# Optimization experiments

Measured on AMD Instinct MI355X. Metric: run time of the kernel, lower is better.

The kernel has to match this reference:

```python
import jax, jax.numpy as jnp
import numpy as np

D = 128  # input_depth == output_depth
NUM_NODES_PATTERN = np.tile(np.array([32, 48, 64, 96], dtype=np.int64), 64)  # G=256 graphs


def _build_indices(nn_np):
    """Per pair-entry (row-major within each n_g x n_g block): global row node,
    global col node, graph id, diagonal mask; plus per-node graph id / size."""
    G = len(nn_np)
    offs = np.zeros(G, dtype=np.int64)
    offs[1:] = np.cumsum(nn_np)[:-1]
    rows_l, cols_l, g_l, diag_l = [], [], [], []
    for gi, (n, o) in enumerate(zip(nn_np, offs)):
        i = np.repeat(np.arange(n, dtype=np.int64), n)  # row index within block
        j = np.tile(np.arange(n, dtype=np.int64), n)    # col index within block
        rows_l.append(o + i)
        cols_l.append(o + j)
        g_l.append(np.full(n * n, gi, dtype=np.int64))
        diag_l.append(i == j)
    rows = np.concatenate(rows_l)
    cols = np.concatenate(cols_l)
    g_edge = np.concatenate(g_l)
    diag = np.concatenate(diag_l)
    g_node = np.repeat(np.arange(G, dtype=np.int64), nn_np)  # graph of each node
    n_node = np.repeat(nn_np, nn_np)                          # n_g of each node
    N = int(nn_np.sum())
    return rows, cols, g_edge, diag, g_node, n_node, N, G


def setup_inputs() -> dict:
    key = jax.random.key(0)
    nn_np = NUM_NODES_PATTERN
    E = int(np.sum(nn_np ** 2))  # 1,064,960 pair entries
    N = int(nn_np.sum())         # 15,360 nodes
    k1, k2, k3 = jax.random.split(key, 3)
    x = jax.random.normal(k1, (E, D), dtype=jnp.float32)
    coeffs = jax.random.normal(k2, (D, D, 5), dtype=jnp.float32) * float(np.sqrt(2.0) / (D + D))
    bias = jnp.zeros((1, D), dtype=jnp.float32)
    edges_index = jax.random.randint(k3, (2, E), 0, N, dtype=jnp.int64)  # unused by the layer
    num_nodes = jnp.asarray(nn_np)
    return {"x": x, "coeffs": coeffs, "bias": bias,
            "edges_index": edges_index, "num_nodes": num_nodes}


def reference(x, coeffs, bias, edges_index, num_nodes):
    # edges_index is unused, matching the original forward.
    nn_np = np.asarray(num_nodes)
    rows, cols, g_edge, diag, g_node, n_node, N, G = _build_indices(nn_np)
    seg = jax.ops.segment_sum
    diag_m = jnp.asarray(diag)[:, None].astype(x.dtype)  # [E,1]
    n = jnp.asarray(n_node).astype(x.dtype)[:, None]     # [N,1] block size per node

    op1 = seg(x * diag_m, jnp.asarray(rows), num_segments=N)          # diag part (unnormalized)
    op3 = seg(x, jnp.asarray(rows), num_segments=N) / n               # row sums / n
    op4 = seg(x, jnp.asarray(cols), num_segments=N) / n               # col sums / n
    diag_g = seg(x * diag_m, jnp.asarray(g_edge), num_segments=G)     # [G,d] trace per graph
    all_g = seg(x, jnp.asarray(g_edge), num_segments=G)               # [G,d] total sum per graph
    gn = jnp.asarray(g_node)
    op2 = diag_g[gn] / n                                              # trace broadcast / n
    op5 = all_g[gn] / (n * n)                                         # total broadcast / n^2

    ops = jnp.stack([op1, op2, op3, op4, op5], axis=2)                # [N, d, 5]
    out = jnp.einsum('dsb,ndb->ns', coeffs, ops) + bias               # [N, output_depth]
    return out
```

## Files before the change

kernel.cpp:

```cpp
#include <hip/hip_runtime.h>

#define D 128


__device__ __forceinline__ void f4add(float4& a, const float4& b) {
    a.x += b.x; a.y += b.y; a.z += b.z; a.w += b.w;
}

__device__ __forceinline__ void f4shflxor_add(float4& a, int mask) {
    a.x += __shfl_xor(a.x, mask);
    a.y += __shfl_xor(a.y, mask);
    a.z += __shfl_xor(a.z, mask);
    a.w += __shfl_xor(a.w, mask);
}

template<int N>
__device__ __forceinline__ void run_class(const float* __restrict__ x,
                                          long ebase, int o, int gidx, int chunk,
                                          float* __restrict__ diagG,
                                          float* __restrict__ rowG,
                                          float* __restrict__ colG,
                                          float* __restrict__ trG,
                                          float* __restrict__ totG,
                                          float4* rowpart ) {
    const int tid = threadIdx.x;
    const int L   = tid & 63;
    const int w   = tid >> 6;
    const int j0  = tid >> 3;
    const int f4  = tid & 7;
    const float invn = 1.0f / (float)N;
    constexpr bool TWO = (N > 64);
    const bool act0 = (j0 < N);
    const bool act1 = TWO && (j0 + 64 < N);

    const float4* x4 = reinterpret_cast<const float4*>(x);
    const long e0 = (ebase + j0) * 32 + chunk * 8 + f4;
    const long e1 = e0 + 64L * 32;
    const long istride = (long)N * 32;

    float4 c0 = {0,0,0,0}, c1 = {0,0,0,0};

    for (int t0 = 0; t0 < N; t0 += 16) {
#pragma unroll 8
        for (int r = 0; r < 16; ++r) {
            const int i = t0 + r;
            float4 v0 = {0,0,0,0}, v1 = {0,0,0,0};
            if (act0) v0 = x4[e0 + (long)i * istride];
            if (TWO && act1) v1 = x4[e1 + (long)i * istride];
            f4add(c0, v0);
            if (TWO) f4add(c1, v1);
            float4 s = v0;
            if (TWO) f4add(s, v1);
            f4shflxor_add(s, 8);
            f4shflxor_add(s, 16);
            f4shflxor_add(s, 32);
            if (L < 8) rowpart[(r * 8 + w) * 8 + L] = s;
        }
        __syncthreads();
        {
            const int r  = tid >> 5;
            const int dd = tid & 31;
            const float* rp = reinterpret_cast<const float*>(rowpart);
            float acc = 0.f;
#pragma unroll
            for (int w2 = 0; w2 < 8; ++w2) acc += rp[r * 256 + w2 * 32 + dd];
            rowG[(long)(o + t0 + r) * D + chunk * 32 + dd] = acc * invn;
        }
        __syncthreads();
    }

    float4 d0 = {0,0,0,0}, d1 = {0,0,0,0};
    if (act0) d0 = x4[e0 + (long)j0 * istride];
    if (TWO && act1) d1 = x4[e1 + (long)(j0 + 64) * istride];

    float4* diag4 = reinterpret_cast<float4*>(diagG);
    float4* col4  = reinterpret_cast<float4*>(colG);
    if (act0) {
        diag4[(long)(o + j0) * 32 + chunk * 8 + f4] = d0;
        col4 [(long)(o + j0) * 32 + chunk * 8 + f4] = c0;
    }
    if (TWO && act1) {
        diag4[(long)(o + j0 + 64) * 32 + chunk * 8 + f4] = d1;
        col4 [(long)(o + j0 + 64) * 32 + chunk * 8 + f4] = c1;
    }

    float4 td = d0; if (TWO) f4add(td, d1);
    float4 tc = c0; if (TWO) f4add(tc, c1);
    f4shflxor_add(td, 8);  f4shflxor_add(tc, 8);
    f4shflxor_add(td, 16); f4shflxor_add(tc, 16);
    f4shflxor_add(td, 32); f4shflxor_add(tc, 32);
    if (L < 8) {
        rowpart[w * 8 + L]      = td;
        rowpart[64 + w * 8 + L] = tc;
    }
    __syncthreads();
    float4* tr4  = reinterpret_cast<float4*>(trG);
    float4* tot4 = reinterpret_cast<float4*>(totG);
    if (tid < 8) {
        float4 a = {0,0,0,0};
#pragma unroll
        for (int w2 = 0; w2 < 8; ++w2) f4add(a, rowpart[w2 * 8 + tid]);
        tr4[gidx * 32 + chunk * 8 + tid] = a;
    } else if (tid < 16) {
        const int f = tid - 8;
        float4 a = {0,0,0,0};
#pragma unroll
        for (int w2 = 0; w2 < 8; ++w2) f4add(a, rowpart[64 + w2 * 8 + f]);
        tot4[gidx * 32 + chunk * 8 + f] = a;
    }
}

__global__ __launch_bounds__(512) void k1_reduce(const float* __restrict__ x,
                                                 float* __restrict__ diagG,
                                                 float* __restrict__ rowG,
                                                 float* __restrict__ colG,
                                                 float* __restrict__ trG,
                                                 float* __restrict__ totG) {
    __shared__ float4 rowpart[1024];

    const int b  = blockIdx.x;
    const int bb = b & 255;
    const int k  = bb >> 2;
    const int chunk = bb & 3;

    if (b < 256) {
        run_class<96>(x, 16640L * k + 7424, 240 * k + 144, 4 * k + 3, chunk, diagG, rowG, colG, trG, totG, rowpart);
    } else if (b < 512) {
        run_class<64>(x, 16640L * k + 3328, 240 * k + 80, 4 * k + 2, chunk, diagG, rowG, colG, trG, totG, rowpart);
    } else if (b < 768) {
        run_class<48>(x, 16640L * k + 1024, 240 * k + 32, 4 * k + 1, chunk, diagG, rowG, colG, trG, totG, rowpart);
    } else {
        run_class<32>(x, 16640L * k, 240 * k, 4 * k, chunk, diagG, rowG, colG, trG, totG, rowpart);
    }
}

__global__ void k0_transpose(const float* __restrict__ coeffs, float* __restrict__ Wt) {
    int d = blockIdx.x;
    int s = threadIdx.x;
    const float* cp = coeffs + ((long)d * D + s) * 5;
#pragma unroll
    for (int b = 0; b < 5; ++b) Wt[b * (D * D) + d * D + s] = cp[b];
}

__global__ __launch_bounds__(128) void k2_pg(const float* __restrict__ trG,
                                             const float* __restrict__ totG,
                                             const float* __restrict__ Wt,
                                             const float* __restrict__ bias,
                                             float* __restrict__ pg) {
    __shared__ float tr[D], tt[D];
    const int ns_[4] = {32, 48, 64, 96};
    int g = blockIdx.x;
    int c = g & 3;
    float invn = 1.0f / (float)ns_[c];

    int s = threadIdx.x;
    tr[s] = trG[g * D + s] * invn;
    tt[s] = totG[g * D + s] * invn * invn;
    __syncthreads();

    const float* W1 = Wt + 1 * D * D;
    const float* W4 = Wt + 4 * D * D;
    float acc = 0.f;
#pragma unroll 4
    for (int dd = 0; dd < D; ++dd)
        acc += W1[dd * D + s] * tr[dd] + W4[dd * D + s] * tt[dd];
    pg[g * D + s] = bias[s] + acc;
}

__global__ __launch_bounds__(512) void k3_gemm(const float* __restrict__ diagG,
                                               const float* __restrict__ rowG,
                                               const float* __restrict__ colG,
                                               const float* __restrict__ Wt,
                                               const float* __restrict__ pg,
                                               float* __restrict__ out) {
    __shared__ float ash[3][64][D];
    __shared__ int gish[64];
    const int nd0 = blockIdx.x * 64;
    const int tid = threadIdx.x;

    for (int idx = tid; idx < 64 * D; idx += 512) {
        int nn = idx >> 7;
        int d  = idx & 127;
        int nd = nd0 + nn;
        int p  = nd / 240;
        int r  = nd - p * 240;
        int c, n;
        if (r < 32)       { c = 0; n = 32; }
        else if (r < 80)  { c = 1; n = 48; }
        else if (r < 144) { c = 2; n = 64; }
        else              { c = 3; n = 96; }
        float invn = 1.0f / (float)n;
        ash[0][nn][d] = diagG[(long)nd * D + d];
        ash[1][nn][d] = rowG[(long)nd * D + d];
        ash[2][nn][d] = colG[(long)nd * D + d] * invn;
        if (d == 0) gish[nn] = 4 * p + c;
    }
    __syncthreads();

    const int s0 = tid & 31;
    const int nq = tid >> 5;
    const float* W0 = Wt;
    const float* W2 = Wt + 2 * D * D;
    const float* W3 = Wt + 3 * D * D;

    float acc[4][4];
#pragma unroll
    for (int a = 0; a < 4; ++a)
#pragma unroll
        for (int ss = 0; ss < 4; ++ss) acc[a][ss] = 0.f;

    for (int d = 0; d < D; ++d) {
        float w0[4], w2[4], w3[4];
#pragma unroll
        for (int ss = 0; ss < 4; ++ss) {
            int s = s0 + 32 * ss;
            w0[ss] = W0[d * D + s];
            w2[ss] = W2[d * D + s];
            w3[ss] = W3[d * D + s];
        }
#pragma unroll
        for (int a = 0; a < 4; ++a) {
            int nn = nq * 4 + a;
            float a0 = ash[0][nn][d];
            float a1 = ash[1][nn][d];
            float a2 = ash[2][nn][d];
#pragma unroll
            for (int ss = 0; ss < 4; ++ss)
                acc[a][ss] += w0[ss] * a0 + w2[ss] * a1 + w3[ss] * a2;
        }
    }

#pragma unroll
    for (int a = 0; a < 4; ++a) {
        int nn = nq * 4 + a;
        int nd = nd0 + nn;
        int g  = gish[nn];
#pragma unroll
        for (int ss = 0; ss < 4; ++ss) {
            int s = s0 + 32 * ss;
            out[(long)nd * D + s] = acc[a][ss] + pg[g * D + s];
        }
    }
}

extern "C" void kernel_launch(void* const* d_in, const int* in_sizes, int n_in,
                              void* d_out, int out_size, void* d_ws, size_t ws_size,
                              hipStream_t stream) {
    const float* x      = (const float*)d_in[0];
    const float* coeffs = (const float*)d_in[1];
    const float* bias   = (const float*)d_in[2];

    float* ws    = (float*)d_ws;
    float* Wt    = ws;
    float* diagG = Wt + 81920;
    float* rowG  = diagG + 1966080;
    float* colG  = rowG + 1966080;
    float* pg    = colG + 1966080;
    float* trG   = pg + 32768;
    float* totG  = trG + 32768;
    float* out   = (float*)d_out;

    k0_transpose<<<128, 128, 0, stream>>>(coeffs, Wt);
    k1_reduce<<<1024, 512, 0, stream>>>(x, diagG, rowG, colG, trG, totG);
    k2_pg<<<256, 128, 0, stream>>>(trG, totG, Wt, bias, pg);
    k3_gemm<<<240, 512, 0, stream>>>(diagG, rowG, colG, Wt, pg, out);
}
```

Baseline: 227.3 us.

## Replace per-tile shuffle row reduction with diagonal-skewed LDS atomic accumulation

Each thread now walks its column starting at the diagonal row and wrapping around, so lanes in a wave touch distinct rows at each step. Row sums are accumulated with shared-memory float atomics into a padded buffer, which removes the cross-lane shuffles and the two block barriers per 16-row tile. The diagonal element is captured on the first iteration. The cost is four LDS atomics per loaded vector and a less contiguous global access pattern across lanes.

```diff
diff --git a/kernel.cpp b/kernel.cpp
--- a/kernel.cpp
+++ b/kernel.cpp
@@ -22,56 +22,80 @@
                                           float* __restrict__ colG,
                                           float* __restrict__ trG,
                                           float* __restrict__ totG,
-                                          float4* rowpart ) {
+                                          float* __restrict__ rowacc ,
+                                          float4* __restrict__ red   ) {
     const int tid = threadIdx.x;
+    const int j0  = tid >> 3;
+    const int f4  = tid & 7;
     const int L   = tid & 63;
     const int w   = tid >> 6;
-    const int j0  = tid >> 3;
-    const int f4  = tid & 7;
-    const float invn = 1.0f / (float)N;
     constexpr bool TWO = (N > 64);
     const bool act0 = (j0 < N);
-    const bool act1 = TWO && (j0 + 64 < N);
+    const bool act1 = TWO && (j0 < 32);
+    const float invn = 1.0f / (float)N;
+
+    for (int idx = tid; idx < N * 33; idx += 512) rowacc[idx] = 0.f;
+    __syncthreads();
 
     const float4* x4 = reinterpret_cast<const float4*>(x);
-    const long e0 = (ebase + j0) * 32 + chunk * 8 + f4;
-    const long e1 = e0 + 64L * 32;
     const long istride = (long)N * 32;
+    const long span    = (long)N * istride;
 
     float4 c0 = {0,0,0,0}, c1 = {0,0,0,0};
-
-    for (int t0 = 0; t0 < N; t0 += 16) {
-#pragma unroll 8
-        for (int r = 0; r < 16; ++r) {
-            const int i = t0 + r;
-            float4 v0 = {0,0,0,0}, v1 = {0,0,0,0};
-            if (act0) v0 = x4[e0 + (long)i * istride];
-            if (TWO && act1) v1 = x4[e1 + (long)i * istride];
-            f4add(c0, v0);
-            if (TWO) f4add(c1, v1);
-            float4 s = v0;
-            if (TWO) f4add(s, v1);
-            f4shflxor_add(s, 8);
-            f4shflxor_add(s, 16);
-            f4shflxor_add(s, 32);
-            if (L < 8) rowpart[(r * 8 + w) * 8 + L] = s;
-        }
-        __syncthreads();
+    float4 d0 = {0,0,0,0}, d1 = {0,0,0,0};
+
+    if (act0) {
+        int i0 = j0;
+        const float4* p0 = x4 + (ebase + (long)j0 * N + j0) * 32 + chunk * 8 + f4;
+        int ro0 = j0 * 33 + f4 * 4;
+        int i1 = 0, ro1 = 0;
+        const float4* p1 = p0;
+        if (TWO && act1) {
+            i1  = j0 + 64;
+            p1  = x4 + (ebase + (long)(j0 + 64) * N + (j0 + 64)) * 32 + chunk * 8 + f4;
+            ro1 = (j0 + 64) * 33 + f4 * 4;
+        }
         {
-            const int r  = tid >> 5;
-            const int dd = tid & 31;
-            const float* rp = reinterpret_cast<const float*>(rowpart);
-            float acc = 0.f;
-#pragma unroll
-            for (int w2 = 0; w2 < 8; ++w2) acc += rp[r * 256 + w2 * 32 + dd];
-            rowG[(long)(o + t0 + r) * D + chunk * 32 + dd] = acc * invn;
-        }
-        __syncthreads();
-    }
-
-    float4 d0 = {0,0,0,0}, d1 = {0,0,0,0};
-    if (act0) d0 = x4[e0 + (long)j0 * istride];
-    if (TWO && act1) d1 = x4[e1 + (long)(j0 + 64) * istride];
+            float4 v = *p0;
+            d0 = v; f4add(c0, v);
+            atomicAdd(&rowacc[ro0 + 0], v.x); atomicAdd(&rowacc[ro0 + 1], v.y);
+            atomicAdd(&rowacc[ro0 + 2], v.z); atomicAdd(&rowacc[ro0 + 3], v.w);
+            ++i0; p0 += istride; ro0 += 33;
+            if (i0 == N) { i0 = 0; p0 -= span; ro0 -= N * 33; }
+            if (TWO && act1) {
+                float4 u = *p1;
+                d1 = u; f4add(c1, u);
+                atomicAdd(&rowacc[ro1 + 0], u.x); atomicAdd(&rowacc[ro1 + 1], u.y);
+                atomicAdd(&rowacc[ro1 + 2], u.z); atomicAdd(&rowacc[ro1 + 3], u.w);
+                ++i1; p1 += istride; ro1 += 33;
+                if (i1 == N) { i1 = 0; p1 -= span; ro1 -= N * 33; }
+            }
+        }
+#pragma unroll 4
+        for (int t = 1; t < N; ++t) {
+            float4 v = *p0;
+            f4add(c0, v);
+            atomicAdd(&rowacc[ro0 + 0], v.x); atomicAdd(&rowacc[ro0 + 1], v.y);
+            atomicAdd(&rowacc[ro0 + 2], v.z); atomicAdd(&rowacc[ro0 + 3], v.w);
+            ++i0; p0 += istride; ro0 += 33;
+            if (i0 == N) { i0 = 0; p0 -= span; ro0 -= N * 33; }
+            if (TWO && act1) {
+                float4 u = *p1;
+                f4add(c1, u);
+                atomicAdd(&rowacc[ro1 + 0], u.x); atomicAdd(&rowacc[ro1 + 1], u.y);
+                atomicAdd(&rowacc[ro1 + 2], u.z); atomicAdd(&rowacc[ro1 + 3], u.w);
+                ++i1; p1 += istride; ro1 += 33;
+                if (i1 == N) { i1 = 0; p1 -= span; ro1 -= N * 33; }
+            }
+        }
+    }
+    __syncthreads();
+
+    for (int idx = tid; idx < N * 32; idx += 512) {
+        const int i  = idx >> 5;
+        const int dd = idx & 31;
+        rowG[(long)(o + i) * D + chunk * 32 + dd] = rowacc[i * 33 + dd] * invn;
+    }
 
     float4* diag4 = reinterpret_cast<float4*>(diagG);
     float4* col4  = reinterpret_cast<float4*>(colG);
@@ -90,8 +114,8 @@
     f4shflxor_add(td, 16); f4shflxor_add(tc, 16);
     f4shflxor_add(td, 32); f4shflxor_add(tc, 32);
     if (L < 8) {
-        rowpart[w * 8 + L]      = td;
-        rowpart[64 + w * 8 + L] = tc;
+        red[w * 8 + L]      = td;
+        red[64 + w * 8 + L] = tc;
     }
     __syncthreads();
     float4* tr4  = reinterpret_cast<float4*>(trG);
@@ -99,13 +123,13 @@
     if (tid < 8) {
         float4 a = {0,0,0,0};
 #pragma unroll
-        for (int w2 = 0; w2 < 8; ++w2) f4add(a, rowpart[w2 * 8 + tid]);
+        for (int w2 = 0; w2 < 8; ++w2) f4add(a, red[w2 * 8 + tid]);
         tr4[gidx * 32 + chunk * 8 + tid] = a;
     } else if (tid < 16) {
         const int f = tid - 8;
         float4 a = {0,0,0,0};
 #pragma unroll
-        for (int w2 = 0; w2 < 8; ++w2) f4add(a, rowpart[64 + w2 * 8 + f]);
+        for (int w2 = 0; w2 < 8; ++w2) f4add(a, red[64 + w2 * 8 + f]);
         tot4[gidx * 32 + chunk * 8 + f] = a;
     }
 }
@@ -116,7 +140,8 @@
                                                  float* __restrict__ colG,
                                                  float* __restrict__ trG,
                                                  float* __restrict__ totG) {
-    __shared__ float4 rowpart[1024];
+    __shared__ float  rowacc[96 * 33];
+    __shared__ float4 red[128];
 
     const int b  = blockIdx.x;
     const int bb = b & 255;
@@ -124,13 +149,13 @@
     const int chunk = bb & 3;
 
     if (b < 256) {
-        run_class<96>(x, 16640L * k + 7424, 240 * k + 144, 4 * k + 3, chunk, diagG, rowG, colG, trG, totG, rowpart);
+        run_class<96>(x, 16640L * k + 7424, 240 * k + 144, 4 * k + 3, chunk, diagG, rowG, colG, trG, totG, rowacc, red);
     } else if (b < 512) {
-        run_class<64>(x, 16640L * k + 3328, 240 * k + 80, 4 * k + 2, chunk, diagG, rowG, colG, trG, totG, rowpart);
+        run_class<64>(x, 16640L * k + 3328, 240 * k + 80, 4 * k + 2, chunk, diagG, rowG, colG, trG, totG, rowacc, red);
     } else if (b < 768) {
-        run_class<48>(x, 16640L * k + 1024, 240 * k + 32, 4 * k + 1, chunk, diagG, rowG, colG, trG, totG, rowpart);
+        run_class<48>(x, 16640L * k + 1024, 240 * k + 32, 4 * k + 1, chunk, diagG, rowG, colG, trG, totG, rowacc, red);
     } else {
-        run_class<32>(x, 16640L * k, 240 * k, 4 * k, chunk, diagG, rowG, colG, trG, totG, rowpart);
+        run_class<32>(x, 16640L * k, 240 * k, 4 * k, chunk, diagG, rowG, colG, trG, totG, rowacc, red);
     }
 }
 
```

After: 774.8 us. +240.9%, slower.
